# Kernel optimization log

Hardware: AMD Instinct MI355X
Metric: run time of the kernel (lower is better)

Reference implementation:

```python
import jax, jax.numpy as jnp
import numpy as np

PRECISION_BITS = 6
NOISE_SCALE = 1.0 / (2 ** (2 * PRECISION_BITS))  # 1/4096, as in call()


def setup_inputs() -> dict:
    key = jax.random.key(0)
    k1, k2, k3, k4, k5 = jax.random.split(key, 5)
    B, D_IN, UNITS = 4096, 4096, 4096
    x = jax.random.normal(k1, (B, D_IN), dtype=jnp.float32)
    kernel = jax.random.normal(k2, (D_IN, UNITS), dtype=jnp.float32) * 0.02
    # per-unit fitted Gaussian params (stats.norm.fit of the convolved error PMF)
    noise_mean = jax.random.normal(k3, (UNITS,), dtype=jnp.float32)
    noise_std = jax.random.uniform(k4, (UNITS,), dtype=jnp.float32)
    # pre-drawn standard-normal variates replacing scipy rvs() for determinism
    noise_eps = jax.random.normal(k5, (B, UNITS), dtype=jnp.float32)
    return {"x": x, "kernel": kernel, "noise_mean": noise_mean,
            "noise_std": noise_std, "noise_eps": noise_eps}


def reference(x, kernel, noise_mean, noise_std, noise_eps):
    # outputs = x @ kernel  ([B, D] @ [D, U] -> [B, U])
    outputs = jnp.matmul(x, kernel)
    # per-unit Gaussian noise: norm(loc=mean[u], scale=std[u]).rvs(B) / 2**(2*pb)
    noise = (noise_mean[None, :] + noise_std[None, :] * noise_eps) * NOISE_SCALE
    outputs = outputs + noise
    # activation is None in this configuration
    return outputs
```

## Files before the change

kernel.cpp:

```cpp
#include <hip/hip_runtime.h>
#include <hip/hip_bf16.h>
#include <stdint.h>

typedef short bf16x8 __attribute__((ext_vector_type(8)));
typedef float f32x4 __attribute__((ext_vector_type(4)));
typedef unsigned short u16x8 __attribute__((ext_vector_type(8)));

#define GLB(p)  ((__attribute__((address_space(1))) void*)(uintptr_t)(p))
#define LDSP(p) ((__attribute__((address_space(3))) void*)(p))

__device__ __forceinline__ void bf16_split(float x, unsigned short& h, unsigned short& l) {
  unsigned u = __float_as_uint(x);
  unsigned hb = (u + 0x7FFFu + ((u >> 16) & 1u)) >> 16;
  h = (unsigned short)hb;
  float d = x - __uint_as_float(hb << 16);
  unsigned u2 = __float_as_uint(d);
  l = (unsigned short)((u2 + 0x7FFFu + ((u2 >> 16) & 1u)) >> 16);
}

__global__ void convert_split_k(const float* __restrict__ in,
                                unsigned short* __restrict__ hi,
                                unsigned short* __restrict__ lo, long n) {
  long i = ((long)blockIdx.x * blockDim.x + threadIdx.x) * 8;
  if (i + 8 > n) return;
  float v[8];
  *(float4*)(&v[0]) = *(const float4*)(in + i);
  *(float4*)(&v[4]) = *(const float4*)(in + i + 4);
  u16x8 vh, vl;
#pragma unroll
  for (int e = 0; e < 8; ++e) {
    unsigned short h, l;
    bf16_split(v[e], h, l);
    vh[e] = h; vl[e] = l;
  }
  *(u16x8*)(hi + i) = vh;
  *(u16x8*)(lo + i) = vl;
}

__global__ void transpose_split_k(const float* __restrict__ in,
                                  unsigned short* __restrict__ hiT,
                                  unsigned short* __restrict__ loT,
                                  int Dk, int U) {
  const int ublocks = U >> 8;
  const int ub = blockIdx.x % ublocks;
  const int db = blockIdx.x / ublocks;
  const int u  = (ub << 8) + threadIdx.x;
  const int d0 = db * 32;
  unsigned short h[32], l[32];
#pragma unroll
  for (int i = 0; i < 32; ++i) {
    float x = in[(long)(d0 + i) * U + u];
    bf16_split(x, h[i], l[i]);
  }
  u16x8* ph = (u16x8*)(hiT + (long)u * Dk + d0);
  u16x8* pl = (u16x8*)(loT + (long)u * Dk + d0);
#pragma unroll
  for (int q = 0; q < 4; ++q) {
    u16x8 vh, vl;
#pragma unroll
    for (int e = 0; e < 8; ++e) { vh[e] = h[q * 8 + e]; vl[e] = l[q * 8 + e]; }
    ph[q] = vh;
    pl[q] = vl;
  }
}

#define BARRIER0 __builtin_amdgcn_s_barrier()
#define WAIT_LGKM0 do { asm volatile("s_waitcnt lgkmcnt(0)" ::: "memory"); \
                        __builtin_amdgcn_sched_barrier(0); } while (0)
#define WAIT_VM0 asm volatile("s_waitcnt vmcnt(0)" ::: "memory")

#define MFMA_BLOCK(IB) do { \
  __builtin_amdgcn_s_setprio(1); \
  _Pragma("unroll") for (int i_ = 0; i_ < 4; ++i_) \
  _Pragma("unroll") for (int j_ = 0; j_ < 4; ++j_) \
    acc[(IB) + i_][j_] = __builtin_amdgcn_mfma_f32_16x16x32_bf16(aF[i_], bF[j_], acc[(IB) + i_][j_], 0, 0, 0); \
  __builtin_amdgcn_s_setprio(0); } while (0)

#define RD_A(HL, HALF) do { \
  _Pragma("unroll") for (int f_ = 0; f_ < 4; ++f_) \
    aF[f_] = *(const bf16x8*)&sA[c][HL][wm * 4096 + (HALF) * 2048 + f_ * 512 + foff]; } while (0)

#define RD_B(HL) do { \
  _Pragma("unroll") for (int f_ = 0; f_ < 4; ++f_) \
    bF[f_] = *(const bf16x8*)&sB[c][HL][wn * 2048 + f_ * 512 + foff]; } while (0)

#define STAGE2(GSRC, LBASE, KOFF) do { \
  __builtin_amdgcn_global_load_lds(GLB((GSRC) + so0 + (KOFF)), LDSP((LBASE) + (wid << 9)), 16, 0, 0); \
  __builtin_amdgcn_global_load_lds(GLB((GSRC) + so1 + (KOFF)), LDSP((LBASE) + 4096 + (wid << 9)), 16, 0, 0); } while (0)

__global__ __launch_bounds__(512, 2) void gemm_bf16x3_8p(
    const unsigned short* __restrict__ Ahi, const unsigned short* __restrict__ Alo,
    const unsigned short* __restrict__ Bhi, const unsigned short* __restrict__ Blo,
    const float* __restrict__ nmean, const float* __restrict__ nstd,
    const float* __restrict__ eps, float* __restrict__ out,
    int M, int N, int K)
{
  __shared__ __align__(16) unsigned short sA[2][2][256 * 32];
  __shared__ __align__(16) unsigned short sB[2][2][256 * 32];

  const int tid  = threadIdx.x;
  const int wid  = tid >> 6;
  const int lane = tid & 63;
  const int l15  = lane & 15;
  const int kg   = lane >> 4;
  const int wm   = wid >> 2;
  const int wn   = wid & 3;

  const int nbm = M >> 8, nbn = N >> 8, nwg = nbm * nbn;
  const int bid = blockIdx.x;
  const int swz = ((nwg & 7) == 0) ? ((bid & 7) * (nwg >> 3) + (bid >> 3)) : bid;
  const int bm = swz % nbm, bn = swz / nbm;
  const long rowA0 = (long)bm << 8;
  const long rowB0 = (long)bn << 8;

  const unsigned short* gAh = Ahi + rowA0 * K;
  const unsigned short* gAl = Alo + rowA0 * K;
  const unsigned short* gBh = Bhi + rowB0 * K;
  const unsigned short* gBl = Blo + rowB0 * K;

  const int e0 = tid, e1 = tid + 512;
  const int r0 = e0 >> 2, r1 = e1 >> 2;
  const long so0 = (long)r0 * K + (long)(((e0 & 3) ^ ((r0 >> 1) & 3)) << 3);
  const long so1 = (long)r1 * K + (long)(((e1 & 3) ^ ((r1 >> 1) & 3)) << 3);

  const int foff = l15 * 32 + ((kg ^ ((l15 >> 1) & 3)) << 3);

  f32x4 acc[8][4];
#pragma unroll
  for (int i = 0; i < 8; ++i)
#pragma unroll
    for (int j = 0; j < 4; ++j) acc[i][j] = (f32x4)0.0f;

  const int nt = K >> 5;

  STAGE2(gAh, &sA[0][0][0], 0);
  STAGE2(gAl, &sA[0][1][0], 0);
  STAGE2(gBh, &sB[0][0][0], 0);
  STAGE2(gBl, &sB[0][1][0], 0);
  WAIT_VM0;
  BARRIER0;

  for (int t = 0; t < nt; ++t) {
    const int c = t & 1;
    const long KOFF = (long)(t + 1) << 5;
    const bool pf = (t + 1 < nt);
    unsigned short* nAh = &sA[c ^ 1][0][0];
    unsigned short* nAl = &sA[c ^ 1][1][0];
    unsigned short* nBh = &sB[c ^ 1][0][0];
    unsigned short* nBl = &sB[c ^ 1][1][0];
    bf16x8 aF[4], bF[4];

    RD_A(0, 0); RD_B(0);
    if (pf) STAGE2(gAh, nAh, KOFF);
    BARRIER0; WAIT_LGKM0; MFMA_BLOCK(0); BARRIER0;

    RD_A(0, 1);
    if (pf) STAGE2(gAl, nAl, KOFF);
    BARRIER0; WAIT_LGKM0; MFMA_BLOCK(4); BARRIER0;

    RD_A(0, 0); RD_B(1);
    if (pf) STAGE2(gBh, nBh, KOFF);
    BARRIER0; WAIT_LGKM0; MFMA_BLOCK(0); BARRIER0;

    RD_A(0, 1);
    if (pf) STAGE2(gBl, nBl, KOFF);
    BARRIER0; WAIT_LGKM0; MFMA_BLOCK(4); BARRIER0;

    RD_A(1, 0); RD_B(0);
    BARRIER0; WAIT_LGKM0; MFMA_BLOCK(0); BARRIER0;

    RD_A(1, 1);
    BARRIER0; WAIT_LGKM0; MFMA_BLOCK(4);
    WAIT_VM0;
    BARRIER0;
  }

  const float NS = 2.44140625e-4f;
  const long r0o = rowA0 + wm * 128;
  const long c0o = rowB0 + wn * 64;
#pragma unroll
  for (int i = 0; i < 8; ++i)
#pragma unroll
    for (int j = 0; j < 4; ++j) {
      const long col = c0o + j * 16 + l15;
      const float mn = nmean[col];
      const float sd = nstd[col];
#pragma unroll
      for (int r = 0; r < 4; ++r) {
        const long row = r0o + i * 16 + kg * 4 + r;
        const long o = row * N + col;
        out[o] = acc[i][j][r] + (mn + sd * eps[o]) * NS;
      }
    }
}

__global__ __launch_bounds__(1024) void fb_gemm(
    const float* __restrict__ A, const float* __restrict__ B,
    const float* __restrict__ nmean, const float* __restrict__ nstd,
    const float* __restrict__ eps, float* __restrict__ out,
    int M, int N, int K) {
  __shared__ float sA[32][33];
  __shared__ float sB[32][33];
  const int tx = threadIdx.x & 31, ty = threadIdx.x >> 5;
  const int row = blockIdx.y * 32 + ty;
  const int col = blockIdx.x * 32 + tx;
  float acc = 0.f;
  for (int kt = 0; kt < K; kt += 32) {
    sA[ty][tx] = A[(long)row * K + kt + tx];
    sB[ty][tx] = B[(long)(kt + ty) * N + col];
    __syncthreads();
#pragma unroll
    for (int k = 0; k < 32; ++k) acc += sA[ty][k] * sB[k][tx];
    __syncthreads();
  }
  const long o = (long)row * N + col;
  out[o] = acc + (nmean[col] + nstd[col] * eps[o]) * 2.44140625e-4f;
}

extern "C" void kernel_launch(void* const* d_in, const int* in_sizes, int n_in,
                              void* d_out, int out_size, void* d_ws, size_t ws_size,
                              hipStream_t stream) {
  (void)n_in; (void)out_size;
  const float* x     = (const float*)d_in[0];
  const float* w     = (const float*)d_in[1];
  const float* nmean = (const float*)d_in[2];
  const float* nstd  = (const float*)d_in[3];
  const float* eps   = (const float*)d_in[4];
  float* out = (float*)d_out;

  const int U  = in_sizes[2];
  const int Dk = in_sizes[1] / U;
  const int Bm = in_sizes[0] / Dk;

  const size_t elemsA = (size_t)Bm * Dk;
  const size_t elemsB = (size_t)Dk * U;
  const size_t need = 2 * (elemsA + elemsB) * sizeof(unsigned short);

  const bool ok = (ws_size >= need) &&
                  (Bm % 256 == 0) && (U % 256 == 0) && (Dk % 32 == 0) &&
                  ((elemsA % 8) == 0);

  if (ok) {
    unsigned short* Ahi  = (unsigned short*)d_ws;
    unsigned short* Alo  = Ahi + elemsA;
    unsigned short* BhiT = Alo + elemsA;
    unsigned short* BloT = BhiT + elemsB;
    const long nA = (long)elemsA;
    const int gridA = (int)((nA / 8 + 255) / 256);
    convert_split_k<<<gridA, 256, 0, stream>>>(x, Ahi, Alo, nA);
    transpose_split_k<<<(U >> 8) * (Dk / 32), 256, 0, stream>>>(w, BhiT, BloT, Dk, U);
    const int nwg = (Bm >> 8) * (U >> 8);
    gemm_bf16x3_8p<<<nwg, 512, 0, stream>>>(Ahi, Alo, BhiT, BloT,
                                            nmean, nstd, eps, out, Bm, U, Dk);
  } else {
    dim3 g(U / 32, Bm / 32);
    fb_gemm<<<g, 1024, 0, stream>>>(x, w, nmean, nstd, eps, out, Bm, U, Dk);
  }
}
```

Measured before the change: 568.9 us.

## Collapse GEMM k-step into two phases and tile weight transpose through LDS

```diff
diff --git a/kernel.cpp b/kernel.cpp
--- a/kernel.cpp
+++ b/kernel.cpp
@@ -37,30 +37,34 @@
   *(u16x8*)(lo + i) = vl;
 }
 
-__global__ void transpose_split_k(const float* __restrict__ in,
-                                  unsigned short* __restrict__ hiT,
-                                  unsigned short* __restrict__ loT,
-                                  int Dk, int U) {
-  const int ublocks = U >> 8;
-  const int ub = blockIdx.x % ublocks;
-  const int db = blockIdx.x / ublocks;
-  const int u  = (ub << 8) + threadIdx.x;
-  const int d0 = db * 32;
-  unsigned short h[32], l[32];
-#pragma unroll
-  for (int i = 0; i < 32; ++i) {
-    float x = in[(long)(d0 + i) * U + u];
-    bf16_split(x, h[i], l[i]);
-  }
-  u16x8* ph = (u16x8*)(hiT + (long)u * Dk + d0);
-  u16x8* pl = (u16x8*)(loT + (long)u * Dk + d0);
-#pragma unroll
-  for (int q = 0; q < 4; ++q) {
-    u16x8 vh, vl;
-#pragma unroll
-    for (int e = 0; e < 8; ++e) { vh[e] = h[q * 8 + e]; vl[e] = l[q * 8 + e]; }
-    ph[q] = vh;
-    pl[q] = vl;
+__global__ __launch_bounds__(256) void transpose_split_k(
+    const float* __restrict__ in, unsigned short* __restrict__ hiT,
+    unsigned short* __restrict__ loT, int Dk, int U) {
+  __shared__ unsigned short lh[16][264];
+  __shared__ unsigned short ll[16][264];
+  const int t = threadIdx.x;
+  const int ublocks = U >> 4;
+  const int u0 = (blockIdx.x % ublocks) << 4;
+  const int d0 = (blockIdx.x / ublocks) << 8;
+  const int ul = t & 15, dl0 = t >> 4;
+#pragma unroll
+  for (int p = 0; p < 16; ++p) {
+    const int d = dl0 + p * 16;
+    float x = in[(long)(d0 + d) * U + (u0 + ul)];
+    unsigned short h, l;
+    bf16_split(x, h, l);
+    lh[ul][d] = h;
+    ll[ul][d] = l;
+  }
+  __syncthreads();
+  const int ur = t >> 5, ck = t & 31;
+#pragma unroll
+  for (int p = 0; p < 2; ++p) {
+    const int u = ur + p * 8;
+    u16x8 vh = *(const u16x8*)&lh[u][ck * 8];
+    u16x8 vl = *(const u16x8*)&ll[u][ck * 8];
+    *(u16x8*)(hiT + (long)(u0 + u) * Dk + d0 + ck * 8) = vh;
+    *(u16x8*)(loT + (long)(u0 + u) * Dk + d0 + ck * 8) = vl;
   }
 }
 
@@ -69,26 +73,28 @@
                         __builtin_amdgcn_sched_barrier(0); } while (0)
 #define WAIT_VM0 asm volatile("s_waitcnt vmcnt(0)" ::: "memory")
 
-#define MFMA_BLOCK(IB) do { \
+#define MFMA_BLOCK3(IB) do { \
   __builtin_amdgcn_s_setprio(1); \
   _Pragma("unroll") for (int i_ = 0; i_ < 4; ++i_) \
   _Pragma("unroll") for (int j_ = 0; j_ < 4; ++j_) \
-    acc[(IB) + i_][j_] = __builtin_amdgcn_mfma_f32_16x16x32_bf16(aF[i_], bF[j_], acc[(IB) + i_][j_], 0, 0, 0); \
+    acc[(IB)+i_][j_] = __builtin_amdgcn_mfma_f32_16x16x32_bf16(aFh[i_], bFh[j_], acc[(IB)+i_][j_], 0, 0, 0); \
+  _Pragma("unroll") for (int i_ = 0; i_ < 4; ++i_) \
+  _Pragma("unroll") for (int j_ = 0; j_ < 4; ++j_) \
+    acc[(IB)+i_][j_] = __builtin_amdgcn_mfma_f32_16x16x32_bf16(aFh[i_], bFl[j_], acc[(IB)+i_][j_], 0, 0, 0); \
+  _Pragma("unroll") for (int i_ = 0; i_ < 4; ++i_) \
+  _Pragma("unroll") for (int j_ = 0; j_ < 4; ++j_) \
+    acc[(IB)+i_][j_] = __builtin_amdgcn_mfma_f32_16x16x32_bf16(aFl[i_], bFh[j_], acc[(IB)+i_][j_], 0, 0, 0); \
   __builtin_amdgcn_s_setprio(0); } while (0)
 
-#define RD_A(HL, HALF) do { \
+#define RD4(DST, BASE, OFS) do { \
   _Pragma("unroll") for (int f_ = 0; f_ < 4; ++f_) \
-    aF[f_] = *(const bf16x8*)&sA[c][HL][wm * 4096 + (HALF) * 2048 + f_ * 512 + foff]; } while (0)
-
-#define RD_B(HL) do { \
-  _Pragma("unroll") for (int f_ = 0; f_ < 4; ++f_) \
-    bF[f_] = *(const bf16x8*)&sB[c][HL][wn * 2048 + f_ * 512 + foff]; } while (0)
+    DST[f_] = *(const bf16x8*)&(BASE)[(OFS) + f_ * 512 + foff]; } while (0)
 
 #define STAGE2(GSRC, LBASE, KOFF) do { \
   __builtin_amdgcn_global_load_lds(GLB((GSRC) + so0 + (KOFF)), LDSP((LBASE) + (wid << 9)), 16, 0, 0); \
   __builtin_amdgcn_global_load_lds(GLB((GSRC) + so1 + (KOFF)), LDSP((LBASE) + 4096 + (wid << 9)), 16, 0, 0); } while (0)
 
-__global__ __launch_bounds__(512, 2) void gemm_bf16x3_8p(
+__global__ __launch_bounds__(512, 2) void gemm_bf16x3_2p(
     const unsigned short* __restrict__ Ahi, const unsigned short* __restrict__ Alo,
     const unsigned short* __restrict__ Bhi, const unsigned short* __restrict__ Blo,
     const float* __restrict__ nmean, const float* __restrict__ nstd,
@@ -148,29 +154,23 @@
     unsigned short* nAl = &sA[c ^ 1][1][0];
     unsigned short* nBh = &sB[c ^ 1][0][0];
     unsigned short* nBl = &sB[c ^ 1][1][0];
-    bf16x8 aF[4], bF[4];
-
-    RD_A(0, 0); RD_B(0);
-    if (pf) STAGE2(gAh, nAh, KOFF);
-    BARRIER0; WAIT_LGKM0; MFMA_BLOCK(0); BARRIER0;
-
-    RD_A(0, 1);
-    if (pf) STAGE2(gAl, nAl, KOFF);
-    BARRIER0; WAIT_LGKM0; MFMA_BLOCK(4); BARRIER0;
-
-    RD_A(0, 0); RD_B(1);
-    if (pf) STAGE2(gBh, nBh, KOFF);
-    BARRIER0; WAIT_LGKM0; MFMA_BLOCK(0); BARRIER0;
-
-    RD_A(0, 1);
-    if (pf) STAGE2(gBl, nBl, KOFF);
-    BARRIER0; WAIT_LGKM0; MFMA_BLOCK(4); BARRIER0;
-
-    RD_A(1, 0); RD_B(0);
-    BARRIER0; WAIT_LGKM0; MFMA_BLOCK(0); BARRIER0;
-
-    RD_A(1, 1);
-    BARRIER0; WAIT_LGKM0; MFMA_BLOCK(4);
+    bf16x8 aFh[4], aFl[4], bFh[4], bFl[4];
+
+    RD4(bFh, sB[c][0], wn * 2048);
+    RD4(bFl, sB[c][1], wn * 2048);
+    RD4(aFh, sA[c][0], wm * 4096);
+    RD4(aFl, sA[c][1], wm * 4096);
+    if (pf) {
+      STAGE2(gAh, nAh, KOFF);
+      STAGE2(gAl, nAl, KOFF);
+      STAGE2(gBh, nBh, KOFF);
+      STAGE2(gBl, nBl, KOFF);
+    }
+    BARRIER0; WAIT_LGKM0; MFMA_BLOCK3(0); BARRIER0;
+
+    RD4(aFh, sA[c][0], wm * 4096 + 2048);
+    RD4(aFl, sA[c][1], wm * 4096 + 2048);
+    BARRIER0; WAIT_LGKM0; MFMA_BLOCK3(4);
     WAIT_VM0;
     BARRIER0;
   }
@@ -237,7 +237,7 @@
   const size_t need = 2 * (elemsA + elemsB) * sizeof(unsigned short);
 
   const bool ok = (ws_size >= need) &&
-                  (Bm % 256 == 0) && (U % 256 == 0) && (Dk % 32 == 0) &&
+                  (Bm % 256 == 0) && (U % 256 == 0) && (Dk % 256 == 0) &&
                   ((elemsA % 8) == 0);
 
   if (ok) {
@@ -248,9 +248,9 @@
     const long nA = (long)elemsA;
     const int gridA = (int)((nA / 8 + 255) / 256);
     convert_split_k<<<gridA, 256, 0, stream>>>(x, Ahi, Alo, nA);
-    transpose_split_k<<<(U >> 8) * (Dk / 32), 256, 0, stream>>>(w, BhiT, BloT, Dk, U);
+    transpose_split_k<<<(U >> 4) * (Dk >> 8), 256, 0, stream>>>(w, BhiT, BloT, Dk, U);
     const int nwg = (Bm >> 8) * (U >> 8);
-    gemm_bf16x3_8p<<<nwg, 512, 0, stream>>>(Ahi, Alo, BhiT, BloT,
+    gemm_bf16x3_2p<<<nwg, 512, 0, stream>>>(Ahi, Alo, BhiT, BloT,
                                             nmean, nstd, eps, out, Bm, U, Dk);
   } else {
     dim3 g(U / 32, Bm / 32);
```

New measurement: 538.7 us. -5.3%, faster.
